# Performance work log

Hardware: AMD Instinct MI355X
Metric: run time of the kernel (lower is better)

The kernel has to match this reference:

```python
import jax, jax.numpy as jnp
import numpy as np

B = 4096
I = 2048  # input_size
H = 2048  # hidden_size


def setup_inputs() -> dict:
    key = jax.random.key(0)
    ks = jax.random.split(key, 5)
    # xavier-uniform-ish scale for the stacked weights (fan_in=2048, fan_out=2048)
    w_scale = np.sqrt(2.0 / (I + H)).astype(np.float32)
    return {
        "x": jax.random.normal(ks[0], (B, I), dtype=jnp.float32),
        "h": jax.random.normal(ks[1], (B, H), dtype=jnp.float32),
        "c": jax.random.normal(ks[2], (B, H), dtype=jnp.float32),
        # stacked gate weights in order [i, f, g, o], each block [H, in]
        "W_x": jax.random.normal(ks[3], (4 * H, I), dtype=jnp.float32) * w_scale,
        "b_x": jnp.zeros((4 * H,), dtype=jnp.float32),
        "W_h": jax.random.normal(ks[4], (4 * H, H), dtype=jnp.float32) * w_scale,
        "b_h": jnp.zeros((4 * H,), dtype=jnp.float32),
    }


def reference(x, h, c, W_x, b_x, W_h, b_h):
    # Two fused GEMMs replace the 8 per-gate nn.Linear calls (same math).
    gates = (
        jnp.einsum("bi,gi->bg", x, W_x)
        + jnp.einsum("bh,gh->bg", h, W_h)
        + b_x
        + b_h
    )  # [B, 4H], gate order i, f, g, o
    i_t, f_t, g_t, o_t = jnp.split(gates, 4, axis=-1)
    i_t = jax.nn.sigmoid(i_t)
    f_t = jax.nn.sigmoid(f_t)
    o_t = jax.nn.sigmoid(o_t)
    g_t = jnp.tanh(g_t)
    c_new = f_t * c + i_t * g_t
    h_new = o_t * jnp.tanh(c_new)
    return (h_new, c_new)
```

## Files before the change

### kernel.cpp

```cpp
#include <hip/hip_runtime.h>
#include <hip/hip_bf16.h>
#include <stdint.h>


typedef float        f32x4 __attribute__((ext_vector_type(4)));
typedef short        s16x8 __attribute__((ext_vector_type(8)));
typedef unsigned int u32x4 __attribute__((ext_vector_type(4)));
typedef unsigned int u32x2 __attribute__((ext_vector_type(2)));
typedef unsigned short ushort_t;

#define BH_TOT 8388608
#define NT 128
#define ALO_B 33554432
#define WLO_B 67108864

__device__ __forceinline__ void splitf4(f32x4 v, u32x2& hp, u32x2& lp) {
  unsigned int u0 = __float_as_uint(v[0]), u1 = __float_as_uint(v[1]);
  unsigned int u2 = __float_as_uint(v[2]), u3 = __float_as_uint(v[3]);
  float d0 = v[0] - __uint_as_float(u0 & 0xFFFF0000u);
  float d1 = v[1] - __uint_as_float(u1 & 0xFFFF0000u);
  float d2 = v[2] - __uint_as_float(u2 & 0xFFFF0000u);
  float d3 = v[3] - __uint_as_float(u3 & 0xFFFF0000u);
  hp[0] = (u0 >> 16) | (u1 & 0xFFFF0000u);
  hp[1] = (u2 >> 16) | (u3 & 0xFFFF0000u);
  unsigned int l0 = __float_as_uint(d0), l1 = __float_as_uint(d1);
  unsigned int l2 = __float_as_uint(d2), l3 = __float_as_uint(d3);
  lp[0] = (l0 >> 16) | (l1 & 0xFFFF0000u);
  lp[1] = (l2 >> 16) | (l3 & 0xFFFF0000u);
}

__device__ __forceinline__ float sigmoidf_(float x) {
  return 1.0f / (1.0f + __expf(-x));
}

__global__ __launch_bounds__(256) void conv_split2(
    const float* __restrict__ srcA, const float* __restrict__ srcB,
    ushort_t* __restrict__ dhi, ushort_t* __restrict__ dlo, int nGroups) {
  const int stride = gridDim.x * blockDim.x;
  for (int g = blockIdx.x * blockDim.x + threadIdx.x; g < nGroups; g += stride) {
    const int row = g >> 9;
    const int gi = g & 511;
    const int half = gi >> 8;
    const int c8 = (gi & 255) << 3;
    const float* s = (half ? srcB : srcA) + (size_t)row * 2048 + c8;
    f32x4 v0 = *(const f32x4*)s;
    f32x4 v1 = *(const f32x4*)(s + 4);
    u32x2 h0, l0, h1, l1;
    splitf4(v0, h0, l0);
    splitf4(v1, h1, l1);
    u32x4 hv = {h0[0], h0[1], h1[0], h1[1]};
    u32x4 lv = {l0[0], l0[1], l1[0], l1[1]};
    const size_t off = (size_t)row * 4096 + half * 2048 + c8;
    *(u32x4*)(dhi + off) = hv;
    *(u32x4*)(dlo + off) = lv;
  }
}

__device__ __forceinline__ void glds16(const void* g, void* l) {
  __builtin_amdgcn_global_load_lds(
      (const __attribute__((address_space(1))) unsigned int*)g,
      (__attribute__((address_space(3))) unsigned int*)l, 16, 0, 0);
}

__device__ __forceinline__ s16x8 ldfrag(const ushort_t* plane, int row, int kq) {
  const int slot = kq ^ ((row >> 1) & 3);
  return *(const s16x8*)(plane + row * 32 + slot * 8);
}

#define VMCNT2 asm volatile("s_waitcnt vmcnt(2)" ::: "memory")
#define BARRIER asm volatile("s_barrier" ::: "memory")

#define MFMA16(A_, B_, R_)                                                  \
  do {                                                                      \
    _Pragma("unroll") for (int tm_ = 0; tm_ < 4; ++tm_)                     \
        _Pragma("unroll") for (int tn_ = 0; tn_ < 4; ++tn_)                 \
            acc[(R_) + tm_][tn_] = __builtin_amdgcn_mfma_f32_16x16x32_bf16( \
                A_[tm_], B_[tn_], acc[(R_) + tm_][tn_], 0, 0, 0);           \
  } while (0)

#define CLUSTER(A1_, B1_, R1_, A2_, B2_, R2_) \
  do {                                        \
    __builtin_amdgcn_s_setprio(1);            \
    MFMA16(A1_, B1_, R1_);                    \
    MFMA16(A2_, B2_, R2_);                    \
    __builtin_amdgcn_s_setprio(0);            \
  } while (0)

#define GLA(extra, plo)                                        \
  do {                                                         \
    glds16(srcA0 + (extra) + ko, bn_ + (plo) + wld);           \
    glds16(srcA1 + (extra) + ko, bn_ + (plo) + 8192 + wld);    \
  } while (0)
#define GLW(extra, plo)                                        \
  do {                                                         \
    glds16(srcW0 + (extra) + ko, bn_ + (plo) + wld);           \
    glds16(srcW1 + (extra) + ko, bn_ + (plo) + 8192 + wld);    \
  } while (0)

__global__ __launch_bounds__(512, 2) void lstm_gemm(
    const ushort_t* __restrict__ Whi, const ushort_t* __restrict__ Ahi,
    const float* __restrict__ cold, const float* __restrict__ bx,
    const float* __restrict__ bh, float* __restrict__ out) {
  __shared__ unsigned char smem[131072];

  const int tid = threadIdx.x;
  const int lane = tid & 63;
  const int wid = tid >> 6;
  const int wg = wid & 3;
  const int wm = wid >> 2;
  const int m16 = lane & 15;
  const int kq = lane >> 4;

  const int swz = (blockIdx.x & 7) * 64 + (blockIdx.x >> 3);
  const int bm0 = (swz >> 5) * 256;
  const int col0 = (swz & 31) * 64;

  const int lrow = tid >> 2;
  const int lslot = tid & 3;
  const int gsl = (lslot ^ ((lrow >> 1) & 3)) << 4;
  const char* Ab = (const char*)Ahi;
  const char* Wb = (const char*)Whi;
  const char* srcA0 = Ab + (size_t)(bm0 + lrow) * 8192 + gsl;
  const char* srcA1 = Ab + (size_t)(bm0 + 128 + lrow) * 8192 + gsl;
  const int wr0 = (lrow >> 6) * 2048 + col0 + (lrow & 63);
  const int wr1 = wr0 + 2 * 2048;
  const char* srcW0 = Wb + (size_t)wr0 * 8192 + gsl;
  const char* srcW1 = Wb + (size_t)wr1 * 8192 + gsl;

  const int wld = wid * 1024;

  f32x4 acc[8][4] = {};

  {
    unsigned char* bn_ = smem;
    const int ko = 0;
    GLA(0, 0);
    GLW(0, 32768);
    GLA(ALO_B, 16384);
    GLW(WLO_B, 49152);
  }
  VMCNT2;
  BARRIER;

  for (int t = 0; t < NT; ++t) {
    const int cb = t & 1;
    unsigned char* bc_ = smem + cb * 65536;
    unsigned char* bn_ = smem + (cb ^ 1) * 65536;
    const int ktn = (t + 1 < NT) ? t + 1 : t;
    const int ko = ktn << 6;
    const ushort_t* pAh = (const ushort_t*)(bc_);
    const ushort_t* pAl = (const ushort_t*)(bc_ + 16384);
    const ushort_t* pWh = (const ushort_t*)(bc_ + 32768);
    const ushort_t* pWl = (const ushort_t*)(bc_ + 49152);
    const int ra = wm * 128;
    s16x8 wh[4], wl[4], a0[4], a1[4], a0p[4], a1p[4];

#pragma unroll
    for (int i = 0; i < 4; ++i) wh[i] = ldfrag(pWh, wg * 64 + i * 16 + m16, kq);
#pragma unroll
    for (int i = 0; i < 4; ++i) a0[i] = ldfrag(pAh, ra + i * 16 + m16, kq);
#pragma unroll
    for (int i = 0; i < 4; ++i) a1[i] = ldfrag(pAl, ra + i * 16 + m16, kq);
    GLA(0, 0);
    VMCNT2;
    BARRIER;
    CLUSTER(a0, wh, 0, a1, wh, 0);
    BARRIER;

#pragma unroll
    for (int i = 0; i < 4; ++i) wl[i] = ldfrag(pWl, wg * 64 + i * 16 + m16, kq);
#pragma unroll
    for (int i = 0; i < 4; ++i)
      a0p[i] = ldfrag(pAh, ra + 64 + i * 16 + m16, kq);
    GLW(0, 32768);
    GLA(ALO_B, 16384);
    BARRIER;
    CLUSTER(a0, wl, 0, a0p, wh, 4);
    BARRIER;

#pragma unroll
    for (int i = 0; i < 4; ++i)
      a1p[i] = ldfrag(pAl, ra + 64 + i * 16 + m16, kq);
    GLW(WLO_B, 49152);
    VMCNT2;
    BARRIER;
    CLUSTER(a1p, wh, 4, a0p, wl, 4);
    BARRIER;
  }

  __syncthreads();
  float* gl = (float*)smem;
  const int colg = tid & 15;
  const int rr = tid >> 4;
  const int cgl = col0 + colg * 4;
  f32x4 bi = *(const f32x4*)(bx + cgl) + *(const f32x4*)(bh + cgl);
  f32x4 bf_ = *(const f32x4*)(bx + 2048 + cgl) + *(const f32x4*)(bh + 2048 + cgl);
  f32x4 bg = *(const f32x4*)(bx + 4096 + cgl) + *(const f32x4*)(bh + 4096 + cgl);
  f32x4 bo = *(const f32x4*)(bx + 6144 + cgl) + *(const f32x4*)(bh + 6144 + cgl);

#pragma unroll
  for (int hh = 0; hh < 2; ++hh) {
    if (hh) __syncthreads();
    if (wm == hh) {
#pragma unroll
      for (int tm = 0; tm < 8; ++tm)
#pragma unroll
        for (int tn = 0; tn < 4; ++tn) {
          const int r = tm * 16 + kq * 4;
          const int c = tn * 16 + m16;
#pragma unroll
          for (int i = 0; i < 4; ++i)
            gl[wg * 8192 + (r + i) * 64 + c] = acc[tm][tn][i];
        }
    }
    __syncthreads();
#pragma unroll
    for (int j = 0; j < 4; ++j) {
      const int r = rr + j * 32;
      f32x4 gi = *(const f32x4*)&gl[0 * 8192 + r * 64 + colg * 4] + bi;
      f32x4 gf = *(const f32x4*)&gl[1 * 8192 + r * 64 + colg * 4] + bf_;
      f32x4 gg = *(const f32x4*)&gl[2 * 8192 + r * 64 + colg * 4] + bg;
      f32x4 go = *(const f32x4*)&gl[3 * 8192 + r * 64 + colg * 4] + bo;
      const size_t gbase = (size_t)(bm0 + hh * 128 + r) * 2048 + cgl;
      f32x4 cv = *(const f32x4*)(cold + gbase);
      f32x4 cn, hn;
#pragma unroll
      for (int e = 0; e < 4; ++e) {
        float iv = sigmoidf_(gi[e]);
        float fv = sigmoidf_(gf[e]);
        float gv = tanhf(gg[e]);
        float ov = sigmoidf_(go[e]);
        float c2 = fv * cv[e] + iv * gv;
        cn[e] = c2;
        hn[e] = ov * tanhf(c2);
      }
      *(f32x4*)(out + gbase) = hn;
      *(f32x4*)(out + BH_TOT + gbase) = cn;
    }
  }
}

__device__ __forceinline__ void splitw(f32x4 w0, f32x4 w1, s16x8& hi, s16x8& lo) {
  u32x2 h0, l0, h1, l1;
  splitf4(w0, h0, l0);
  splitf4(w1, h1, l1);
  u32x4 hu = {h0[0], h0[1], h1[0], h1[1]};
  u32x4 lu = {l0[0], l0[1], l1[0], l1[1]};
  hi = __builtin_bit_cast(s16x8, hu);
  lo = __builtin_bit_cast(s16x8, lu);
}

__global__ __launch_bounds__(256, 2) void lstm_fused(
    const float* __restrict__ x, const float* __restrict__ h,
    const float* __restrict__ cold, const float* __restrict__ Wx,
    const float* __restrict__ bx, const float* __restrict__ Wh,
    const float* __restrict__ bh, float* __restrict__ out) {
  __shared__ unsigned char smem[69632];
  ushort_t* Ah = (ushort_t*)smem;
  ushort_t* Al = (ushort_t*)(smem + 5120);
  float* gl = (float*)smem;

  const int tid = threadIdx.x;
  const int lane = tid & 63;
  const int wid = tid >> 6;

  const int swz = (blockIdx.x & 7) * 256 + (blockIdx.x >> 3);
  const int bn = swz >> 6;
  const int bm = swz & 63;
  const int row0 = bm * 64;
  const int col0 = bn * 64;

  const int ar0 = tid >> 3;
  const int akc = (tid & 7) << 2;
  const int wcol = lane & 15;
  const int kch = (lane >> 4) << 3;

  f32x4 acc[4][4];
#pragma unroll
  for (int i = 0; i < 4; ++i)
#pragma unroll
    for (int j = 0; j < 4; ++j) acc[i][j] = (f32x4)0.0f;

#pragma unroll
  for (int ph = 0; ph < 2; ++ph) {
    const float* Ap = ph ? h : x;
    const float* Wp = ph ? Wh : Wx;
    const float* arow0 = Ap + (size_t)(row0 + ar0) * 2048 + akc;
    const float* arow1 = arow0 + 32 * 2048;
    const float* wb[4];
#pragma unroll
    for (int tn = 0; tn < 4; ++tn)
      wb[tn] = Wp + (size_t)(wid * 2048 + col0 + tn * 16 + wcol) * 2048 + kch;

    f32x4 a0 = *(const f32x4*)(arow0);
    f32x4 a1 = *(const f32x4*)(arow1);

    for (int kt = 0; kt < 64; ++kt) {
      const int k0 = kt << 5;
      f32x4 wr[4][2];
#pragma unroll
      for (int tn = 0; tn < 4; ++tn) {
        wr[tn][0] = *(const f32x4*)(wb[tn] + k0);
        wr[tn][1] = *(const f32x4*)(wb[tn] + k0 + 4);
      }
      {
        u32x2 hp, lp;
        splitf4(a0, hp, lp);
        *(u32x2*)(Ah + ar0 * 40 + akc) = hp;
        *(u32x2*)(Al + ar0 * 40 + akc) = lp;
        splitf4(a1, hp, lp);
        *(u32x2*)(Ah + (ar0 + 32) * 40 + akc) = hp;
        *(u32x2*)(Al + (ar0 + 32) * 40 + akc) = lp;
      }
      __syncthreads();
      if (kt != 63) {
        a0 = *(const f32x4*)(arow0 + k0 + 32);
        a1 = *(const f32x4*)(arow1 + k0 + 32);
      }
      s16x8 ah[4], al[4];
#pragma unroll
      for (int tm = 0; tm < 4; ++tm) {
        const int off = (tm * 16 + wcol) * 40 + kch;
        ah[tm] = *(const s16x8*)(Ah + off);
        al[tm] = *(const s16x8*)(Al + off);
      }
      s16x8 whh[4], wll[4];
#pragma unroll
      for (int tn = 0; tn < 4; ++tn) splitw(wr[tn][0], wr[tn][1], whh[tn], wll[tn]);
#pragma unroll
      for (int tm = 0; tm < 4; ++tm)
#pragma unroll
        for (int tn = 0; tn < 4; ++tn)
          acc[tm][tn] = __builtin_amdgcn_mfma_f32_16x16x32_bf16(
              ah[tm], whh[tn], acc[tm][tn], 0, 0, 0);
#pragma unroll
      for (int tm = 0; tm < 4; ++tm)
#pragma unroll
        for (int tn = 0; tn < 4; ++tn)
          acc[tm][tn] = __builtin_amdgcn_mfma_f32_16x16x32_bf16(
              ah[tm], wll[tn], acc[tm][tn], 0, 0, 0);
#pragma unroll
      for (int tm = 0; tm < 4; ++tm)
#pragma unroll
        for (int tn = 0; tn < 4; ++tn)
          acc[tm][tn] = __builtin_amdgcn_mfma_f32_16x16x32_bf16(
              al[tm], whh[tn], acc[tm][tn], 0, 0, 0);
      __syncthreads();
    }
  }

  {
    const int rbase = (lane >> 4) << 2;
#pragma unroll
    for (int tm = 0; tm < 4; ++tm)
#pragma unroll
      for (int tn = 0; tn < 4; ++tn) {
        const int r = tm * 16 + rbase;
        const int cc = tn * 16 + wcol;
#pragma unroll
        for (int i = 0; i < 4; ++i)
          gl[wid * 4352 + (r + i) * 68 + cc] = acc[tm][tn][i];
      }
  }
  __syncthreads();

  const int ecol = (tid & 15) << 2;
  const int er0 = tid >> 4;
  const int cg = col0 + ecol;
  f32x4 bi = *(const f32x4*)(bx + cg) + *(const f32x4*)(bh + cg);
  f32x4 bf = *(const f32x4*)(bx + 2048 + cg) + *(const f32x4*)(bh + 2048 + cg);
  f32x4 bg = *(const f32x4*)(bx + 4096 + cg) + *(const f32x4*)(bh + 4096 + cg);
  f32x4 bo = *(const f32x4*)(bx + 6144 + cg) + *(const f32x4*)(bh + 6144 + cg);
#pragma unroll
  for (int j = 0; j < 4; ++j) {
    const int r = er0 + j * 16;
    const size_t gbase = (size_t)(row0 + r) * 2048 + cg;
    f32x4 gi = *(const f32x4*)&gl[0 * 4352 + r * 68 + ecol] + bi;
    f32x4 gf = *(const f32x4*)&gl[1 * 4352 + r * 68 + ecol] + bf;
    f32x4 gg = *(const f32x4*)&gl[2 * 4352 + r * 68 + ecol] + bg;
    f32x4 go = *(const f32x4*)&gl[3 * 4352 + r * 68 + ecol] + bo;
    f32x4 cv = *(const f32x4*)(cold + gbase);
    f32x4 cn, hn;
#pragma unroll
    for (int e = 0; e < 4; ++e) {
      float iv = sigmoidf_(gi[e]);
      float fv = sigmoidf_(gf[e]);
      float gv = tanhf(gg[e]);
      float ov = sigmoidf_(go[e]);
      float c2 = fv * cv[e] + iv * gv;
      cn[e] = c2;
      hn[e] = ov * tanhf(c2);
    }
    *(f32x4*)(out + gbase) = hn;
    *(f32x4*)(out + BH_TOT + gbase) = cn;
  }
}

extern "C" void kernel_launch(void* const* d_in, const int* in_sizes, int n_in,
                              void* d_out, int out_size, void* d_ws,
                              size_t ws_size, hipStream_t stream) {
  const float* x = (const float*)d_in[0];
  const float* h = (const float*)d_in[1];
  const float* c = (const float*)d_in[2];
  const float* Wx = (const float*)d_in[3];
  const float* bx = (const float*)d_in[4];
  const float* Wh = (const float*)d_in[5];
  const float* bh = (const float*)d_in[6];
  float* out = (float*)d_out;

  const size_t NEED = 201326592ULL;
  if (ws_size >= NEED) {
    ushort_t* base = (ushort_t*)d_ws;
    ushort_t* Whi = base;
    ushort_t* Wlo = base + 33554432;
    ushort_t* Ahi = base + 67108864;
    ushort_t* Alo = base + 83886080;
    hipLaunchKernelGGL(conv_split2, dim3(4096), dim3(256), 0, stream, Wx, Wh,
                       Whi, Wlo, 8192 * 512);
    hipLaunchKernelGGL(conv_split2, dim3(2048), dim3(256), 0, stream, x, h,
                       Ahi, Alo, 4096 * 512);
    hipLaunchKernelGGL(lstm_gemm, dim3(512), dim3(512), 0, stream, Whi, Ahi, c,
                       bx, bh, out);
  } else {
    hipLaunchKernelGGL(lstm_fused, dim3(2048), dim3(256), 0, stream, x, h, c,
                       Wx, bx, Wh, bh, out);
  }
}
```

Measured before the change: 893.1 us.

## Merge conversion kernels and simplify GEMM K-loop to one barrier per step

The two fp32-to-bf16 hi/lo split launches are merged into a single grid-stride kernel covering the weights and the activations, which removes one launch. In the GEMM main loop, all four global-to-LDS prefetches for the next K-step are now issued up front. The staggered vmcnt(2) waits and the multiple barriers are replaced by a single vmcnt(0) plus one barrier at the end of each iteration. This cuts barrier and synchronisation overhead, but the full drain waits for every load before the next step and may expose memory latency that the staged scheme used to hide.

After: 911.8 us. 2.1% more time.

```diff
diff --git a/kernel.cpp b/kernel.cpp
--- a/kernel.cpp
+++ b/kernel.cpp
@@ -33,16 +33,30 @@
   return 1.0f / (1.0f + __expf(-x));
 }
 
-__global__ __launch_bounds__(256) void conv_split2(
-    const float* __restrict__ srcA, const float* __restrict__ srcB,
-    ushort_t* __restrict__ dhi, ushort_t* __restrict__ dlo, int nGroups) {
+__global__ __launch_bounds__(256) void conv_all(
+    const float* __restrict__ Wx, const float* __restrict__ Wh,
+    const float* __restrict__ x, const float* __restrict__ h,
+    ushort_t* __restrict__ Whi, ushort_t* __restrict__ Wlo,
+    ushort_t* __restrict__ Ahi, ushort_t* __restrict__ Alo) {
   const int stride = gridDim.x * blockDim.x;
-  for (int g = blockIdx.x * blockDim.x + threadIdx.x; g < nGroups; g += stride) {
-    const int row = g >> 9;
-    const int gi = g & 511;
-    const int half = gi >> 8;
-    const int c8 = (gi & 255) << 3;
-    const float* s = (half ? srcB : srcA) + (size_t)row * 2048 + c8;
+  for (int g = blockIdx.x * blockDim.x + threadIdx.x; g < 6291456; g += stride) {
+    const float* s;
+    ushort_t *dh, *dl;
+    size_t off;
+    if (g < 4194304) {
+      const int row = g >> 9, gi = g & 511;
+      const int half = gi >> 8, c8 = (gi & 255) << 3;
+      s = (half ? Wh : Wx) + (size_t)row * 2048 + c8;
+      off = (size_t)row * 4096 + half * 2048 + c8;
+      dh = Whi; dl = Wlo;
+    } else {
+      const int ga = g - 4194304;
+      const int row = ga >> 9, gi = ga & 511;
+      const int half = gi >> 8, c8 = (gi & 255) << 3;
+      s = (half ? h : x) + (size_t)row * 2048 + c8;
+      off = (size_t)row * 4096 + half * 2048 + c8;
+      dh = Ahi; dl = Alo;
+    }
     f32x4 v0 = *(const f32x4*)s;
     f32x4 v1 = *(const f32x4*)(s + 4);
     u32x2 h0, l0, h1, l1;
@@ -50,9 +64,8 @@
     splitf4(v1, h1, l1);
     u32x4 hv = {h0[0], h0[1], h1[0], h1[1]};
     u32x4 lv = {l0[0], l0[1], l1[0], l1[1]};
-    const size_t off = (size_t)row * 4096 + half * 2048 + c8;
-    *(u32x4*)(dhi + off) = hv;
-    *(u32x4*)(dlo + off) = lv;
+    *(u32x4*)(dh + off) = hv;
+    *(u32x4*)(dl + off) = lv;
   }
 }
 
@@ -67,7 +80,7 @@
   return *(const s16x8*)(plane + row * 32 + slot * 8);
 }
 
-#define VMCNT2 asm volatile("s_waitcnt vmcnt(2)" ::: "memory")
+#define VMCNT0 asm volatile("s_waitcnt vmcnt(0)" ::: "memory")
 #define BARRIER asm volatile("s_barrier" ::: "memory")
 
 #define MFMA16(A_, B_, R_)                                                  \
@@ -139,7 +152,7 @@
     GLA(ALO_B, 16384);
     GLW(WLO_B, 49152);
   }
-  VMCNT2;
+  VMCNT0;
   BARRIER;
 
   for (int t = 0; t < NT; ++t) {
@@ -155,36 +168,32 @@
     const int ra = wm * 128;
     s16x8 wh[4], wl[4], a0[4], a1[4], a0p[4], a1p[4];
 
+    GLA(0, 0);
+    GLW(0, 32768);
+    GLA(ALO_B, 16384);
+    GLW(WLO_B, 49152);
+
 #pragma unroll
     for (int i = 0; i < 4; ++i) wh[i] = ldfrag(pWh, wg * 64 + i * 16 + m16, kq);
 #pragma unroll
     for (int i = 0; i < 4; ++i) a0[i] = ldfrag(pAh, ra + i * 16 + m16, kq);
 #pragma unroll
     for (int i = 0; i < 4; ++i) a1[i] = ldfrag(pAl, ra + i * 16 + m16, kq);
-    GLA(0, 0);
-    VMCNT2;
-    BARRIER;
     CLUSTER(a0, wh, 0, a1, wh, 0);
-    BARRIER;
 
 #pragma unroll
     for (int i = 0; i < 4; ++i) wl[i] = ldfrag(pWl, wg * 64 + i * 16 + m16, kq);
 #pragma unroll
     for (int i = 0; i < 4; ++i)
       a0p[i] = ldfrag(pAh, ra + 64 + i * 16 + m16, kq);
-    GLW(0, 32768);
-    GLA(ALO_B, 16384);
-    BARRIER;
     CLUSTER(a0, wl, 0, a0p, wh, 4);
-    BARRIER;
 
 #pragma unroll
     for (int i = 0; i < 4; ++i)
       a1p[i] = ldfrag(pAl, ra + 64 + i * 16 + m16, kq);
-    GLW(WLO_B, 49152);
-    VMCNT2;
-    BARRIER;
     CLUSTER(a1p, wh, 4, a0p, wl, 4);
+
+    VMCNT0;
     BARRIER;
   }
 
@@ -415,10 +424,8 @@
     ushort_t* Wlo = base + 33554432;
     ushort_t* Ahi = base + 67108864;
     ushort_t* Alo = base + 83886080;
-    hipLaunchKernelGGL(conv_split2, dim3(4096), dim3(256), 0, stream, Wx, Wh,
-                       Whi, Wlo, 8192 * 512);
-    hipLaunchKernelGGL(conv_split2, dim3(2048), dim3(256), 0, stream, x, h,
-                       Ahi, Alo, 4096 * 512);
+    hipLaunchKernelGGL(conv_all, dim3(2048), dim3(256), 0, stream, Wx, Wh, x,
+                       h, Whi, Wlo, Ahi, Alo);
     hipLaunchKernelGGL(lstm_gemm, dim3(512), dim3(512), 0, stream, Whi, Ahi, c,
                        bx, bh, out);
   } else {
```
